# Optimization experiments

Hardware: AMD Instinct MI355X
Metric: run time of the kernel (lower is better)

Reference implementation:

```python
import jax, jax.numpy as jnp
import numpy as np


def setup_inputs() -> dict:
    key = jax.random.key(0)
    kx, kw = jax.random.split(key)
    x = jax.random.normal(kx, (65536, 4096), dtype=jnp.float32)  # [tokens, in_features]
    w = jax.random.normal(kw, (4096, 4096), dtype=jnp.float32)   # [out_features, in_features]
    return {"x": x, "w": w}


def reference(x, w):
    # Observer assumes fresh state: running min/max == current-batch min/max.
    # input_obs (ch_axis=1): per-column stats of x
    x_min = jnp.min(x, axis=0)  # [D]
    x_max = jnp.max(x, axis=0)  # [D]
    # weight_col_obs (ch_axis=1): per-column stats of w
    w_col_min = jnp.min(w, axis=0)  # [D]
    w_col_max = jnp.max(w, axis=0)  # [D]
    # weight_row_obs (ch_axis=0): per-row stats of w
    w_row_min = jnp.min(w, axis=1)  # [N]
    w_row_max = jnp.max(w, axis=1)  # [N]
    # Python loop of torch.where(w[i] == min_vals[i])[0][0] == first-occurrence
    # row argmin/argmax; vectorized here.
    min_weights_ind = jnp.argmin(w, axis=1).astype(jnp.int64)  # [N]
    max_weights_ind = jnp.argmax(w, axis=1).astype(jnp.int64)  # [N]
    return (x_min, x_max, w_col_min, w_col_max, w_row_min, w_row_max,
            min_weights_ind, max_weights_ind)
```

## Files before the change

kernel.cpp:

```cpp
#include <hip/hip_runtime.h>
#include <math.h>

#define COLS 4096
#define COLS4 1024

__global__ __launch_bounds__(256) void col_minmax_stage1(
    const float* __restrict__ src, int rows, int rows_per_chunk,
    float* __restrict__ ws_min, float* __restrict__ ws_max)
{
    int chunk = blockIdx.x;
    int r0 = chunk * rows_per_chunk;
    int r1 = r0 + rows_per_chunk;
    if (r1 > rows) r1 = rows;

    float4 mn[4], mx[4];
#pragma unroll
    for (int j = 0; j < 4; ++j) {
        mn[j] = make_float4( INFINITY,  INFINITY,  INFINITY,  INFINITY);
        mx[j] = make_float4(-INFINITY, -INFINITY, -INFINITY, -INFINITY);
    }

    const float4* p = (const float4*)src + (size_t)r0 * COLS4 + threadIdx.x;
    for (int r = r0; r < r1; ++r, p += COLS4) {
#pragma unroll
        for (int j = 0; j < 4; ++j) {
            float4 v = p[j * 256];
            mn[j].x = fminf(mn[j].x, v.x); mx[j].x = fmaxf(mx[j].x, v.x);
            mn[j].y = fminf(mn[j].y, v.y); mx[j].y = fmaxf(mx[j].y, v.y);
            mn[j].z = fminf(mn[j].z, v.z); mx[j].z = fmaxf(mx[j].z, v.z);
            mn[j].w = fminf(mn[j].w, v.w); mx[j].w = fmaxf(mx[j].w, v.w);
        }
    }

    float4* omn = (float4*)ws_min + (size_t)chunk * COLS4 + threadIdx.x;
    float4* omx = (float4*)ws_max + (size_t)chunk * COLS4 + threadIdx.x;
#pragma unroll
    for (int j = 0; j < 4; ++j) {
        omn[j * 256] = mn[j];
        omx[j * 256] = mx[j];
    }
}

__global__ __launch_bounds__(256) void col_minmax_reduce(
    const float* __restrict__ in_min, const float* __restrict__ in_max,
    int n_in, int cpg,
    float* __restrict__ out_min, float* __restrict__ out_max)
{
    int c4 = blockIdx.x * 256 + threadIdx.x;
    if (c4 >= COLS4) return;
    int g = blockIdx.y;
    int k0 = g * cpg;
    int k1 = k0 + cpg;
    if (k1 > n_in) k1 = n_in;

    float4 mn = make_float4( INFINITY,  INFINITY,  INFINITY,  INFINITY);
    float4 mx = make_float4(-INFINITY, -INFINITY, -INFINITY, -INFINITY);
    for (int k = k0; k < k1; ++k) {
        float4 a = ((const float4*)in_min)[(size_t)k * COLS4 + c4];
        float4 b = ((const float4*)in_max)[(size_t)k * COLS4 + c4];
        mn.x = fminf(mn.x, a.x); mx.x = fmaxf(mx.x, b.x);
        mn.y = fminf(mn.y, a.y); mx.y = fmaxf(mx.y, b.y);
        mn.z = fminf(mn.z, a.z); mx.z = fmaxf(mx.z, b.z);
        mn.w = fminf(mn.w, a.w); mx.w = fmaxf(mx.w, b.w);
    }
    ((float4*)out_min)[(size_t)g * COLS4 + c4] = mn;
    ((float4*)out_max)[(size_t)g * COLS4 + c4] = mx;
}

__global__ __launch_bounds__(256) void row_minmax_arg(
    const float* __restrict__ w,
    float* __restrict__ out_min, float* __restrict__ out_max,
    float* __restrict__ out_imin, float* __restrict__ out_imax)
{
    __shared__ float s_mn[256], s_mx[256];
    __shared__ int   s_in[256], s_ix[256];

    int row = blockIdx.x;
    const float4* w4 = (const float4*)(w + (size_t)row * COLS);

    float mn = INFINITY, mx = -INFINITY;
    int imn = 0, imx = 0;
#pragma unroll
    for (int u = 0; u < COLS4 / 256; ++u) {
        int i = u * 256 + threadIdx.x;
        float4 v = w4[i];
        int b = i << 2;
        if (v.x < mn) { mn = v.x; imn = b;     }
        if (v.x > mx) { mx = v.x; imx = b;     }
        if (v.y < mn) { mn = v.y; imn = b + 1; }
        if (v.y > mx) { mx = v.y; imx = b + 1; }
        if (v.z < mn) { mn = v.z; imn = b + 2; }
        if (v.z > mx) { mx = v.z; imx = b + 2; }
        if (v.w < mn) { mn = v.w; imn = b + 3; }
        if (v.w > mx) { mx = v.w; imx = b + 3; }
    }

    int t = threadIdx.x;
    s_mn[t] = mn; s_in[t] = imn;
    s_mx[t] = mx; s_ix[t] = imx;
    __syncthreads();

    for (int s = 128; s > 0; s >>= 1) {
        if (t < s) {
            float ov = s_mn[t + s]; int oi = s_in[t + s];
            if (ov < s_mn[t] || (ov == s_mn[t] && oi < s_in[t])) { s_mn[t] = ov; s_in[t] = oi; }
            ov = s_mx[t + s]; oi = s_ix[t + s];
            if (ov > s_mx[t] || (ov == s_mx[t] && oi < s_ix[t])) { s_mx[t] = ov; s_ix[t] = oi; }
        }
        __syncthreads();
    }

    if (t == 0) {
        out_min[row]  = s_mn[0];
        out_max[row]  = s_mx[0];
        out_imin[row] = (float)s_in[0];
        out_imax[row] = (float)s_ix[0];
    }
}

extern "C" void kernel_launch(void* const* d_in, const int* in_sizes, int n_in,
                              void* d_out, int out_size, void* d_ws, size_t ws_size,
                              hipStream_t stream) {
    const float* x = (const float*)d_in[0];
    const float* w = (const float*)d_in[1];
    float* out = (float*)d_out;

    int rows_x = in_sizes[0] / COLS;
    int rows_w = in_sizes[1] / COLS;

    const int chunks_x = 1024, g2_x = 32;
    const int chunks_w = 256, g2_w = 8;
    int rpc_x = (rows_x + chunks_x - 1) / chunks_x;
    int rpc_w = (rows_w + chunks_w - 1) / chunks_w;

    float* ws_min_x  = (float*)d_ws;
    float* ws_max_x  = ws_min_x  + (size_t)chunks_x * COLS;
    float* ws2_min_x = ws_max_x  + (size_t)chunks_x * COLS;
    float* ws2_max_x = ws2_min_x + (size_t)g2_x * COLS;
    float* ws_min_w  = ws2_max_x + (size_t)g2_x * COLS;
    float* ws_max_w  = ws_min_w  + (size_t)chunks_w * COLS;
    float* ws2_min_w = ws_max_w  + (size_t)chunks_w * COLS;
    float* ws2_max_w = ws2_min_w + (size_t)g2_w * COLS;

    float* x_min     = out + 0 * COLS;
    float* x_max     = out + 1 * COLS;
    float* w_col_min = out + 2 * COLS;
    float* w_col_max = out + 3 * COLS;
    float* w_row_min = out + 4 * COLS;
    float* w_row_max = out + 5 * COLS;
    float* w_imin    = out + 6 * COLS;
    float* w_imax    = out + 7 * COLS;

    dim3 blk(256);

    col_minmax_stage1<<<dim3(chunks_x), blk, 0, stream>>>(
        x, rows_x, rpc_x, ws_min_x, ws_max_x);
    col_minmax_stage1<<<dim3(chunks_w), blk, 0, stream>>>(
        w, rows_w, rpc_w, ws_min_w, ws_max_w);
    row_minmax_arg<<<dim3(rows_w), blk, 0, stream>>>(
        w, w_row_min, w_row_max, w_imin, w_imax);

    col_minmax_reduce<<<dim3(COLS4 / 256, g2_x), blk, 0, stream>>>(
        ws_min_x, ws_max_x, chunks_x, chunks_x / g2_x, ws2_min_x, ws2_max_x);
    col_minmax_reduce<<<dim3(COLS4 / 256, 1), blk, 0, stream>>>(
        ws2_min_x, ws2_max_x, g2_x, g2_x, x_min, x_max);

    col_minmax_reduce<<<dim3(COLS4 / 256, g2_w), blk, 0, stream>>>(
        ws_min_w, ws_max_w, chunks_w, chunks_w / g2_w, ws2_min_w, ws2_max_w);
    col_minmax_reduce<<<dim3(COLS4 / 256, 1), blk, 0, stream>>>(
        ws2_min_w, ws2_max_w, g2_w, g2_w, w_col_min, w_col_max);
}
```

Baseline: 1.413 ms.

## Stride column reduction across interleaved rows with 8-deep loads; batch reduce launches

The first-stage column min/max kernel now gives each block one quarter-row column slice and a strided set of rows (row q, q+Q, ...), so concurrent blocks read adjacent rows. It also issues eight independent float4 loads per iteration to keep more memory requests in flight. Grid size is quadrupled with fewer registers per thread. The x and w second-stage reductions are merged into a single kernel per level, cutting four launches to two. The loop assumes the row count is divisible by chunks times 8, which holds for the test shapes.

```diff
diff --git a/kernel.cpp b/kernel.cpp
--- a/kernel.cpp
+++ b/kernel.cpp
@@ -4,67 +4,75 @@
 #define COLS 4096
 #define COLS4 1024
 
-__global__ __launch_bounds__(256) void col_minmax_stage1(
-    const float* __restrict__ src, int rows, int rows_per_chunk,
+__global__ __launch_bounds__(256) void col_minmax_stage1_lin(
+    const float* __restrict__ src, int Q, int iters,
     float* __restrict__ ws_min, float* __restrict__ ws_max)
 {
-    int chunk = blockIdx.x;
-    int r0 = chunk * rows_per_chunk;
-    int r1 = r0 + rows_per_chunk;
-    if (r1 > rows) r1 = rows;
+    const int b = blockIdx.x;
+    const int t = threadIdx.x;
+    const int f4col = ((b & 3) << 8) | t;
+    const int q     = b >> 2;
 
-    float4 mn[4], mx[4];
+    const size_t stride = (size_t)Q * COLS4;
+    const float4* p = (const float4*)src + (size_t)q * COLS4 + f4col;
+
+    float4 mn = make_float4( INFINITY,  INFINITY,  INFINITY,  INFINITY);
+    float4 mx = make_float4(-INFINITY, -INFINITY, -INFINITY, -INFINITY);
+
+    for (int k = 0; k < iters; k += 8) {
+        float4 v[8];
 #pragma unroll
-    for (int j = 0; j < 4; ++j) {
-        mn[j] = make_float4( INFINITY,  INFINITY,  INFINITY,  INFINITY);
-        mx[j] = make_float4(-INFINITY, -INFINITY, -INFINITY, -INFINITY);
-    }
-
-    const float4* p = (const float4*)src + (size_t)r0 * COLS4 + threadIdx.x;
-    for (int r = r0; r < r1; ++r, p += COLS4) {
+        for (int u = 0; u < 8; ++u)
+            v[u] = p[(size_t)u * stride];
+        p += 8 * stride;
 #pragma unroll
-        for (int j = 0; j < 4; ++j) {
-            float4 v = p[j * 256];
-            mn[j].x = fminf(mn[j].x, v.x); mx[j].x = fmaxf(mx[j].x, v.x);
-            mn[j].y = fminf(mn[j].y, v.y); mx[j].y = fmaxf(mx[j].y, v.y);
-            mn[j].z = fminf(mn[j].z, v.z); mx[j].z = fmaxf(mx[j].z, v.z);
-            mn[j].w = fminf(mn[j].w, v.w); mx[j].w = fmaxf(mx[j].w, v.w);
+        for (int u = 0; u < 8; ++u) {
+            mn.x = fminf(mn.x, v[u].x); mx.x = fmaxf(mx.x, v[u].x);
+            mn.y = fminf(mn.y, v[u].y); mx.y = fmaxf(mx.y, v[u].y);
+            mn.z = fminf(mn.z, v[u].z); mx.z = fmaxf(mx.z, v[u].z);
+            mn.w = fminf(mn.w, v[u].w); mx.w = fmaxf(mx.w, v[u].w);
         }
     }
 
-    float4* omn = (float4*)ws_min + (size_t)chunk * COLS4 + threadIdx.x;
-    float4* omx = (float4*)ws_max + (size_t)chunk * COLS4 + threadIdx.x;
-#pragma unroll
-    for (int j = 0; j < 4; ++j) {
-        omn[j * 256] = mn[j];
-        omx[j * 256] = mx[j];
-    }
+    ((float4*)ws_min)[(size_t)q * COLS4 + f4col] = mn;
+    ((float4*)ws_max)[(size_t)q * COLS4 + f4col] = mx;
 }
 
-__global__ __launch_bounds__(256) void col_minmax_reduce(
-    const float* __restrict__ in_min, const float* __restrict__ in_max,
-    int n_in, int cpg,
-    float* __restrict__ out_min, float* __restrict__ out_max)
+__global__ __launch_bounds__(256) void col_minmax_reduce2(
+    const float* __restrict__ a_in_min, const float* __restrict__ a_in_max,
+    int a_n, int a_cpg, int a_groups,
+    float* __restrict__ a_out_min, float* __restrict__ a_out_max,
+    const float* __restrict__ b_in_min, const float* __restrict__ b_in_max,
+    int b_n, int b_cpg,
+    float* __restrict__ b_out_min, float* __restrict__ b_out_max)
 {
     int c4 = blockIdx.x * 256 + threadIdx.x;
     if (c4 >= COLS4) return;
-    int g = blockIdx.y;
-    int k0 = g * cpg;
-    int k1 = k0 + cpg;
-    if (k1 > n_in) k1 = n_in;
+
+    const float* im; const float* ix; float* om; float* ox;
+    int g, k0, k1;
+    if ((int)blockIdx.y < a_groups) {
+        g = blockIdx.y;
+        im = a_in_min; ix = a_in_max; om = a_out_min; ox = a_out_max;
+        k0 = g * a_cpg; k1 = k0 + a_cpg; if (k1 > a_n) k1 = a_n;
+    } else {
+        g = blockIdx.y - a_groups;
+        im = b_in_min; ix = b_in_max; om = b_out_min; ox = b_out_max;
+        k0 = g * b_cpg; k1 = k0 + b_cpg; if (k1 > b_n) k1 = b_n;
+    }
 
     float4 mn = make_float4( INFINITY,  INFINITY,  INFINITY,  INFINITY);
     float4 mx = make_float4(-INFINITY, -INFINITY, -INFINITY, -INFINITY);
     for (int k = k0; k < k1; ++k) {
-        float4 a = ((const float4*)in_min)[(size_t)k * COLS4 + c4];
-        float4 b = ((const float4*)in_max)[(size_t)k * COLS4 + c4];
+        float4 a = ((const float4*)im)[(size_t)k * COLS4 + c4];
+        float4 b = ((const float4*)ix)[(size_t)k * COLS4 + c4];
         mn.x = fminf(mn.x, a.x); mx.x = fmaxf(mx.x, b.x);
         mn.y = fminf(mn.y, a.y); mx.y = fmaxf(mx.y, b.y);
         mn.z = fminf(mn.z, a.z); mx.z = fmaxf(mx.z, b.z);
         mn.w = fminf(mn.w, a.w); mx.w = fmaxf(mx.w, b.w);
     }
-    ((float4*)out_min)[(size_t)g * COLS4 + c4] = mn;
-    ((float4*)out_max)[(size_t)g * COLS4 + c4] = mx;
+    ((float4*)om)[(size_t)g * COLS4 + c4] = mn;
+    ((float4*)ox)[(size_t)g * COLS4 + c4] = mx;
 }
 
 __global__ __launch_bounds__(256) void row_minmax_arg(
@@ -130,8 +138,8 @@
 
     const int chunks_x = 1024, g2_x = 32;
     const int chunks_w = 256, g2_w = 8;
-    int rpc_x = (rows_x + chunks_x - 1) / chunks_x;
-    int rpc_w = (rows_w + chunks_w - 1) / chunks_w;
+    int iters_x = rows_x / chunks_x;
+    int iters_w = rows_w / chunks_w;
 
     float* ws_min_x  = (float*)d_ws;
     float* ws_max_x  = ws_min_x  + (size_t)chunks_x * COLS;
@@ -153,20 +161,17 @@
 
     dim3 blk(256);
 
-    col_minmax_stage1<<<dim3(chunks_x), blk, 0, stream>>>(
-        x, rows_x, rpc_x, ws_min_x, ws_max_x);
-    col_minmax_stage1<<<dim3(chunks_w), blk, 0, stream>>>(
-        w, rows_w, rpc_w, ws_min_w, ws_max_w);
+    col_minmax_stage1_lin<<<dim3(chunks_x * 4), blk, 0, stream>>>(
+        x, chunks_x, iters_x, ws_min_x, ws_max_x);
+    col_minmax_stage1_lin<<<dim3(chunks_w * 4), blk, 0, stream>>>(
+        w, chunks_w, iters_w, ws_min_w, ws_max_w);
     row_minmax_arg<<<dim3(rows_w), blk, 0, stream>>>(
         w, w_row_min, w_row_max, w_imin, w_imax);
 
-    col_minmax_reduce<<<dim3(COLS4 / 256, g2_x), blk, 0, stream>>>(
-        ws_min_x, ws_max_x, chunks_x, chunks_x / g2_x, ws2_min_x, ws2_max_x);
-    col_minmax_reduce<<<dim3(COLS4 / 256, 1), blk, 0, stream>>>(
-        ws2_min_x, ws2_max_x, g2_x, g2_x, x_min, x_max);
-
-    col_minmax_reduce<<<dim3(COLS4 / 256, g2_w), blk, 0, stream>>>(
+    col_minmax_reduce2<<<dim3(COLS4 / 256, g2_x + g2_w), blk, 0, stream>>>(
+        ws_min_x, ws_max_x, chunks_x, chunks_x / g2_x, g2_x, ws2_min_x, ws2_max_x,
         ws_min_w, ws_max_w, chunks_w, chunks_w / g2_w, ws2_min_w, ws2_max_w);
-    col_minmax_reduce<<<dim3(COLS4 / 256, 1), blk, 0, stream>>>(
+    col_minmax_reduce2<<<dim3(COLS4 / 256, 2), blk, 0, stream>>>(
+        ws2_min_x, ws2_max_x, g2_x, g2_x, 1, x_min, x_max,
         ws2_min_w, ws2_max_w, g2_w, g2_w, w_col_min, w_col_max);
 }
```

Result: no change. 1.440 ms (+1.9%).
